# Kernel tuning notes

Hardware: AMD Instinct MI355X
Metric: run time of the kernel (lower is better)

Reference implementation:

```python
import jax, jax.numpy as jnp
import numpy as np

BN_EPS = 1e-5


def setup_inputs() -> dict:
    N, E, D, L = 100000, 1200000, 64, 3
    key = jax.random.key(0)
    ks = jax.random.split(key, 6)
    x = jax.random.normal(ks[0], (N, D), dtype=jnp.float32)
    src = jax.random.randint(ks[1], (E,), 0, N, dtype=jnp.int32)
    dst = jax.random.randint(ks[2], (E,), 0, N, dtype=jnp.int32)
    W1 = jax.random.normal(ks[3], (L, D, D), dtype=jnp.float32) * 0.1
    W2 = jax.random.normal(ks[4], (L, D, D), dtype=jnp.float32) * 0.1
    b1 = jnp.zeros((L, D), jnp.float32)
    b2 = jnp.zeros((L, D), jnp.float32)
    bn_gamma = jnp.ones((L, D), jnp.float32)
    bn_beta = jnp.zeros((L, D), jnp.float32)
    bn_mean = jnp.zeros((L, D), jnp.float32)
    bn_var = jnp.ones((L, D), jnp.float32)
    return {"x": x, "src": src, "dst": dst, "W1": W1, "b1": b1,
            "bn_gamma": bn_gamma, "bn_beta": bn_beta, "bn_mean": bn_mean,
            "bn_var": bn_var, "W2": W2, "b2": b2}


def reference(x, src, dst, W1, b1, bn_gamma, bn_beta, bn_mean, bn_var, W2, b2):
    # GIN stack, eval mode (dropout is a no-op, BatchNorm uses running stats).
    N = x.shape[0]
    L = W1.shape[0]
    h = x
    jk_sum = jnp.zeros((N, W2.shape[-1]), x.dtype)
    for layer in range(L):  # small fixed layer loop
        # GINConv with eps=0: (1+eps)*x_i + sum_{j->i} x_j
        agg = jax.ops.segment_sum(h[src], dst, num_segments=N)  # [N, D]
        pre = h + agg
        # MLP: Linear -> BatchNorm1d (inference) -> ReLU -> Linear
        z = pre @ W1[layer] + b1[layer]
        z = bn_gamma[layer] * (z - bn_mean[layer]) * jax.lax.rsqrt(bn_var[layer] + BN_EPS) + bn_beta[layer]
        z = jax.nn.relu(z)
        h = z @ W2[layer] + b2[layer]
        if layer != L - 1:
            h = jax.nn.relu(h)  # inter-layer ReLU from the wrapper
        jk_sum = jk_sum + h  # JK='sum' over h_list[1:]
    return jk_sum
```

## Files before the change

### kernel.cpp

```cpp
#include <hip/hip_runtime.h>
#include <hip/hip_fp16.h>

#define NDIM 64
#define RS 68
#define MAXNB 512
#define CAP 6144
#define EBUF 352

typedef _Float16 h4 __attribute__((ext_vector_type(4)));
typedef float f4v __attribute__((ext_vector_type(4)));

__global__ __launch_bounds__(256) void prep_kernel(
    const float* __restrict__ x, __half* __restrict__ x16, int n4,
    const float* __restrict__ W1, const float* __restrict__ b1,
    const float* __restrict__ gamma, const float* __restrict__ beta,
    const float* __restrict__ mean, const float* __restrict__ var,
    const float* __restrict__ W2,
    _Float16* __restrict__ Wpk, float* __restrict__ b1f, int L,
    int* __restrict__ bcnt, int nbz)
{
    int bid = blockIdx.x;
    int t = threadIdx.x;
    if (bid < 2 * L) {
        if (bid == 0)
            for (int i = t; i < nbz; i += 256) bcnt[i] = 0;
        int l = bid >> 1, m = bid & 1;
        const float* Wsrc = (m == 0 ? W1 : W2) + (size_t)l * 4096;
        if (m == 0 && t < 64) {
            float s = gamma[l * 64 + t] * rsqrtf(var[l * 64 + t] + 1e-5f);
            b1f[l * 64 + t] = (b1[l * 64 + t] - mean[l * 64 + t]) * s + beta[l * 64 + t];
        }
        int lane = t & 63;
        int c16 = lane & 15, kq = lane >> 4;
        for (int it = 0; it < 4; ++it) {
            int frag = it * 4 + (t >> 6);
            int ks = frag >> 2, ct = frag & 3;
            int col = ct * 16 + c16;
            int k0 = ks * 16 + kq * 4;
            float s = 1.f;
            if (m == 0) s = gamma[l * 64 + col] * rsqrtf(var[l * 64 + col] + 1e-5f);
            _Float16* dstp = Wpk + (((size_t)(l * 2 + m) * 16 + frag) * 64 + lane) * 8;
            for (int j = 0; j < 4; ++j) {
                float wv = Wsrc[(size_t)(k0 + j) * 64 + col] * s;
                _Float16 hi = (_Float16)wv;
                dstp[j] = hi;
                dstp[4 + j] = (_Float16)(wv - (float)hi);
            }
        }
        return;
    }
    int tid = (bid - 2 * L) * 256 + t;
    if (tid >= n4) return;
    float4 v = *(const float4*)(x + (size_t)tid * 4);
    __half2* dp = (__half2*)(x16 + (size_t)tid * 4);
    dp[0] = __floats2half2_rn(v.x, v.y);
    dp[1] = __floats2half2_rn(v.z, v.w);
}

__global__ __launch_bounds__(256) void bucket_scatter_kernel(
    const int* __restrict__ src, const int* __restrict__ dst,
    int* __restrict__ bcnt, unsigned int* __restrict__ packed, int E, int NBb)
{
    __shared__ int hist[MAXNB];
    __shared__ int sbase[MAXNB];
    for (int i = threadIdx.x; i < NBb; i += 256) hist[i] = 0;
    __syncthreads();
    int start = blockIdx.x * blockDim.x + threadIdx.x;
    int stride = gridDim.x * blockDim.x;
    for (int e = start; e < E; e += stride)
        atomicAdd(&hist[dst[e] >> 8], 1);
    __syncthreads();
    for (int i = threadIdx.x; i < NBb; i += 256) {
        int v = hist[i];
        sbase[i] = v ? (i * CAP + atomicAdd(&bcnt[i], v)) : 0;
    }
    __syncthreads();
    for (int i = threadIdx.x; i < NBb; i += 256) hist[i] = 0;
    __syncthreads();
    for (int e = start; e < E; e += stride) {
        int d = dst[e];
        int b = d >> 8;
        int r = atomicAdd(&hist[b], 1);
        packed[sbase[b] + r] = (unsigned)src[e] | ((unsigned)(d & 255) << 24);
    }
}

__global__ __launch_bounds__(256) void bucket_csr_kernel(
    const unsigned int* __restrict__ packed, const int* __restrict__ bcnt,
    int* __restrict__ ssrc, int* __restrict__ offs, int* __restrict__ ends, int N)
{
    __shared__ int hist[256], scan[256], cur[256];
    __shared__ int swbase;
    int b = blockIdx.x;
    int t = threadIdx.x;
    int partial = 0;
    for (int i = t; i < b; i += 256) partial += bcnt[i];
    scan[t] = partial;
    hist[t] = 0;
    __syncthreads();
    for (int d = 128; d > 0; d >>= 1) {
        if (t < d) scan[t] += scan[t + d];
        __syncthreads();
    }
    if (t == 0) swbase = scan[0];
    __syncthreads();
    int wbase = swbase;
    int cnt = bcnt[b];
    if (cnt > CAP) cnt = CAP;
    size_t rbase = (size_t)b * CAP;
    for (int i = t; i < cnt; i += 256)
        atomicAdd(&hist[packed[rbase + i] >> 24], 1);
    __syncthreads();
    int v = hist[t];
    scan[t] = v;
    __syncthreads();
    for (int d = 1; d < 256; d <<= 1) {
        int x = scan[t];
        int y = (t >= d) ? scan[t - d] : 0;
        __syncthreads();
        scan[t] = x + y;
        __syncthreads();
    }
    int e0 = wbase + scan[t] - v;
    cur[t] = e0;
    int node = b * 256 + t;
    if (node < N) { offs[node] = e0; ends[node] = e0 + v; }
    __syncthreads();
    for (int i = t; i < cnt; i += 256) {
        unsigned p = packed[rbase + i];
        int pos = atomicAdd(&cur[p >> 24], 1);
        ssrc[pos] = (int)(p & 0xFFFFFF);
    }
}

__device__ inline void add4(float4& a, const float4& v) {
    a.x += v.x; a.y += v.y; a.z += v.z; a.w += v.w;
}

__device__ inline void cvt_acc(uint4 u, float4& a0, float4& a1) {
    __half2 h0 = __builtin_bit_cast(__half2, u.x);
    __half2 h1 = __builtin_bit_cast(__half2, u.y);
    __half2 h2 = __builtin_bit_cast(__half2, u.z);
    __half2 h3 = __builtin_bit_cast(__half2, u.w);
    float2 f0 = __half22float2(h0), f1 = __half22float2(h1);
    float2 f2 = __half22float2(h2), f3 = __half22float2(h3);
    a0.x += f0.x; a0.y += f0.y; a0.z += f1.x; a0.w += f1.y;
    a1.x += f2.x; a1.y += f2.y; a1.z += f3.x; a1.w += f3.y;
}

__global__ __launch_bounds__(256, 7) void gin_layer_kernel(
    const __half* __restrict__ hin, __half* __restrict__ hout,
    float* __restrict__ jk, const __half* __restrict__ hbase,
    const int* __restrict__ offs, const int* __restrict__ ends,
    const int* __restrict__ ssrc,
    const _Float16* __restrict__ w1p, const _Float16* __restrict__ w2p,
    const float* __restrict__ b1f, const float* __restrict__ b2,
    int N, int L, int relu_out, int last)
{
    __shared__ float lds[64 * RS];
    __shared__ int ebuf_s[4 * EBUF];
    int t = threadIdx.x;
    int lane = t & 63;
    int w = t >> 6;
    int row0 = blockIdx.x * 64;
    int wrow0 = row0 + w * 16;
    if (wrow0 >= N) return;

    float* wtile = lds + (size_t)w * 16 * RS;
    int* ebuf = ebuf_s + w * EBUF;

    int offv = 0, endv = 0;
    if (lane < 16) {
        int node = wrow0 + lane;
        int cn = (node < N) ? node : (N - 1);
        offv = offs[cn];
        endv = ends[cn];
        if (node >= N) offv = endv;
    }
    int begAll = __shfl(offv, 0, 64);
    int endAll = __shfl(endv, 15, 64);
    int cnt = endAll - begAll;

    bool useLds = (cnt <= EBUF);
    if (useLds) {
        for (int k = lane; k < cnt; k += 64) ebuf[k] = ssrc[begAll + k];
    }
    asm volatile("" ::: "memory");
    auto eidx = [&](int pos) -> int {
        return useLds ? ebuf[pos - begAll] : ssrc[pos];
    };

    {
        int rslot = lane >> 3;
        int q = lane & 7;
        int nodeA = wrow0 + rslot;
        int nodeB = wrow0 + 8 + rslot;
        int begA = __shfl(offv, rslot, 64),     endA = __shfl(endv, rslot, 64);
        int begB = __shfl(offv, 8 + rslot, 64), endB = __shfl(endv, 8 + rslot, 64);

        float4 a0 = make_float4(0.f, 0.f, 0.f, 0.f);
        float4 a1 = make_float4(0.f, 0.f, 0.f, 0.f);
        float4 c0 = make_float4(0.f, 0.f, 0.f, 0.f);
        float4 c1 = make_float4(0.f, 0.f, 0.f, 0.f);
        if (nodeA < N) {
            uint4 u = *(const uint4*)(hin + (size_t)nodeA * NDIM + q * 8);
            cvt_acc(u, a0, a1);
        }
        if (nodeB < N) {
            uint4 u = *(const uint4*)(hin + (size_t)nodeB * NDIM + q * 8);
            cvt_acc(u, c0, c1);
        }
        int kA = begA, kB = begB;
        while (kA + 2 <= endA && kB + 2 <= endB) {
            int iA0 = eidx(kA), iA1 = eidx(kA + 1);
            int iB0 = eidx(kB), iB1 = eidx(kB + 1);
            uint4 uA0 = *(const uint4*)(hin + (size_t)iA0 * NDIM + q * 8);
            uint4 uA1 = *(const uint4*)(hin + (size_t)iA1 * NDIM + q * 8);
            uint4 uB0 = *(const uint4*)(hin + (size_t)iB0 * NDIM + q * 8);
            uint4 uB1 = *(const uint4*)(hin + (size_t)iB1 * NDIM + q * 8);
            cvt_acc(uA0, a0, a1);
            cvt_acc(uA1, a0, a1);
            cvt_acc(uB0, c0, c1);
            cvt_acc(uB1, c0, c1);
            kA += 2; kB += 2;
        }
        for (; kA < endA; ++kA) {
            uint4 u = *(const uint4*)(hin + (size_t)eidx(kA) * NDIM + q * 8);
            cvt_acc(u, a0, a1);
        }
        for (; kB < endB; ++kB) {
            uint4 u = *(const uint4*)(hin + (size_t)eidx(kB) * NDIM + q * 8);
            cvt_acc(u, c0, c1);
        }
        if (nodeA < N) {
            float* p = wtile + rslot * RS + q * 8;
            *(float4*)(p) = a0;
            *(float4*)(p + 4) = a1;
        }
        if (nodeB < N) {
            float* p = wtile + (8 + rslot) * RS + q * 8;
            *(float4*)(p) = c0;
            *(float4*)(p + 4) = c1;
        }
    }
    asm volatile("" ::: "memory");

    int lane15 = lane & 15;
    int lgrp = lane >> 4;
    const float* aRow = wtile + (size_t)lane15 * RS;
    const h4* W1 = (const h4*)w1p;
    const h4* W2 = (const h4*)w2p;
    f4v zero = {0.f, 0.f, 0.f, 0.f};
    f4v acc[4];

    #pragma unroll
    for (int ct = 0; ct < 4; ++ct) acc[ct] = zero;
    #pragma unroll
    for (int ks = 0; ks < 4; ++ks) {
        float4 av = *(const float4*)(aRow + ks * 16 + lgrp * 4);
        h4 ah, al;
        ah[0] = (_Float16)av.x; al[0] = (_Float16)(av.x - (float)ah[0]);
        ah[1] = (_Float16)av.y; al[1] = (_Float16)(av.y - (float)ah[1]);
        ah[2] = (_Float16)av.z; al[2] = (_Float16)(av.z - (float)ah[2]);
        ah[3] = (_Float16)av.w; al[3] = (_Float16)(av.w - (float)ah[3]);
        #pragma unroll
        for (int ct = 0; ct < 4; ++ct) {
            const h4* bp = W1 + (size_t)((ks * 4 + ct) * 64 + lane) * 2;
            h4 bh = bp[0], bl = bp[1];
            acc[ct] = __builtin_amdgcn_mfma_f32_16x16x16f16(ah, bh, acc[ct], 0, 0, 0);
            acc[ct] = __builtin_amdgcn_mfma_f32_16x16x16f16(al, bh, acc[ct], 0, 0, 0);
            acc[ct] = __builtin_amdgcn_mfma_f32_16x16x16f16(ah, bl, acc[ct], 0, 0, 0);
        }
    }
    asm volatile("" ::: "memory");
    #pragma unroll
    for (int ct = 0; ct < 4; ++ct) {
        int col = ct * 16 + lane15;
        float bb = b1f[col];
        #pragma unroll
        for (int i = 0; i < 4; ++i)
            wtile[(size_t)(lgrp * 4 + i) * RS + col] = fmaxf(acc[ct][i] + bb, 0.f);
    }
    asm volatile("" ::: "memory");

    #pragma unroll
    for (int ct = 0; ct < 4; ++ct) acc[ct] = zero;
    #pragma unroll
    for (int ks = 0; ks < 4; ++ks) {
        float4 av = *(const float4*)(aRow + ks * 16 + lgrp * 4);
        h4 ah, al;
        ah[0] = (_Float16)av.x; al[0] = (_Float16)(av.x - (float)ah[0]);
        ah[1] = (_Float16)av.y; al[1] = (_Float16)(av.y - (float)ah[1]);
        ah[2] = (_Float16)av.z; al[2] = (_Float16)(av.z - (float)ah[2]);
        ah[3] = (_Float16)av.w; al[3] = (_Float16)(av.w - (float)ah[3]);
        #pragma unroll
        for (int ct = 0; ct < 4; ++ct) {
            const h4* bp = W2 + (size_t)((ks * 4 + ct) * 64 + lane) * 2;
            h4 bh = bp[0], bl = bp[1];
            acc[ct] = __builtin_amdgcn_mfma_f32_16x16x16f16(ah, bh, acc[ct], 0, 0, 0);
            acc[ct] = __builtin_amdgcn_mfma_f32_16x16x16f16(al, bh, acc[ct], 0, 0, 0);
            acc[ct] = __builtin_amdgcn_mfma_f32_16x16x16f16(ah, bl, acc[ct], 0, 0, 0);
        }
    }
    asm volatile("" ::: "memory");
    #pragma unroll
    for (int ct = 0; ct < 4; ++ct) {
        int col = ct * 16 + lane15;
        float bb = b2[col];
        #pragma unroll
        for (int i = 0; i < 4; ++i) {
            float hv = acc[ct][i] + bb;
            if (relu_out) hv = fmaxf(hv, 0.f);
            wtile[(size_t)(lgrp * 4 + i) * RS + col] = hv;
        }
    }
    asm volatile("" ::: "memory");

    size_t nstride = (size_t)N * NDIM;
    #pragma unroll
    for (int it = 0; it < 4; ++it) {
        int fl = it * 64 + lane;
        int r = fl >> 4, c4 = fl & 15;
        int grow = wrow0 + r;
        if (grow >= N) continue;
        const float* p = wtile + (size_t)r * RS + c4 * 4;
        float4 hv = make_float4(p[0], p[1], p[2], p[3]);
        if (!last) {
            __half2* dp = (__half2*)(hout + (size_t)grow * NDIM + c4 * 4);
            dp[0] = __floats2half2_rn(hv.x, hv.y);
            dp[1] = __floats2half2_rn(hv.z, hv.w);
        } else {
            for (int j = 1; j < L; ++j) {
                uint2 u = *(const uint2*)(hbase + (size_t)j * nstride
                                          + (size_t)grow * NDIM + c4 * 4);
                __half2 x0 = __builtin_bit_cast(__half2, u.x);
                __half2 x1 = __builtin_bit_cast(__half2, u.y);
                float2 f0 = __half22float2(x0), f1 = __half22float2(x1);
                hv.x += f0.x; hv.y += f0.y; hv.z += f1.x; hv.w += f1.y;
            }
            *(float4*)(jk + (size_t)grow * NDIM + c4 * 4) = hv;
        }
    }
}

extern "C" void kernel_launch(void* const* d_in, const int* in_sizes, int n_in,
                              void* d_out, int out_size, void* d_ws, size_t ws_size,
                              hipStream_t stream) {
    const float* x     = (const float*)d_in[0];
    const int*   src   = (const int*)  d_in[1];
    const int*   dst   = (const int*)  d_in[2];
    const float* W1    = (const float*)d_in[3];
    const float* b1    = (const float*)d_in[4];
    const float* gamma = (const float*)d_in[5];
    const float* beta  = (const float*)d_in[6];
    const float* mean  = (const float*)d_in[7];
    const float* var   = (const float*)d_in[8];
    const float* W2    = (const float*)d_in[9];
    const float* b2    = (const float*)d_in[10];

    int N = in_sizes[0] / NDIM;
    int E = in_sizes[1];
    int L = in_sizes[3] / (NDIM * NDIM);
    int NBb = (N + 255) >> 8;
    int n4 = N * NDIM / 4;
    float* out = (float*)d_out;
    size_t ns = (size_t)N * NDIM;

    char* w = (char*)d_ws;
    size_t off = 0;
    auto carve = [&](size_t bytes) -> void* {
        void* p = w + off;
        off += (bytes + 255) & ~(size_t)255;
        return p;
    };
    __half* h16     = (__half*)carve((size_t)(L + 1) * ns * 2);
    int*    ssrc    = (int*)   carve((size_t)E * 4);
    unsigned int* packed = (unsigned int*)carve((size_t)NBb * CAP * 4);
    int*    offs    = (int*)   carve((size_t)N * 4);
    int*    ends    = (int*)   carve((size_t)N * 4);
    int*    bcnt    = (int*)   carve((size_t)(MAXNB + 1) * 4);
    _Float16* Wpk   = (_Float16*)carve((size_t)L * 2 * 16 * 64 * 8 * 2);
    float*  b1f     = (float*) carve((size_t)L * NDIM * 4);

    prep_kernel<<<2 * L + (n4 + 255) / 256, 256, 0, stream>>>(
        x, h16, n4, W1, b1, gamma, beta, mean, var, W2, Wpk, b1f, L,
        bcnt, NBb + 1);
    bucket_scatter_kernel<<<256, 256, 0, stream>>>(src, dst, bcnt, packed, E, NBb);
    bucket_csr_kernel<<<NBb, 256, 0, stream>>>(packed, bcnt, ssrc, offs, ends, N);

    for (int l = 0; l < L; ++l) {
        gin_layer_kernel<<<(N + 63) / 64, 256, 0, stream>>>(
            h16 + (size_t)l * ns, h16 + (size_t)(l + 1) * ns, out, h16,
            offs, ends, ssrc,
            Wpk + (size_t)(l * 2 + 0) * 16 * 64 * 8,
            Wpk + (size_t)(l * 2 + 1) * 16 * 64 * 8,
            b1f + (size_t)l * NDIM, b2 + (size_t)l * NDIM,
            N, L, (l < L - 1) ? 1 : 0, (l == L - 1) ? 1 : 0);
    }
}
```

Measured before the change: 244.4 us.

## Use one-wavefront blocks per 16 rows and unroll gather loop by four

The GIN layer kernel now launches 64-thread blocks that each own 16 rows, instead of 256-thread blocks holding four independent waves. Each block's shared memory shrinks to one wave's tile and edge buffer. This removes tail imbalance inside a block, since a wave no longer waits on its siblings before the block's resources are freed. The neighbor-gather loop is also unrolled to four edges per row pair, with a two-edge remainder, to put more loads in flight. In exchange there are four times as many blocks, and the extra live registers could limit occupancy.

```diff
diff --git a/kernel.cpp b/kernel.cpp
--- a/kernel.cpp
+++ b/kernel.cpp
@@ -148,7 +148,7 @@
     a1.x += f2.x; a1.y += f2.y; a1.z += f3.x; a1.w += f3.y;
 }
 
-__global__ __launch_bounds__(256, 7) void gin_layer_kernel(
+__global__ __launch_bounds__(64, 7) void gin_layer_kernel(
     const __half* __restrict__ hin, __half* __restrict__ hout,
     float* __restrict__ jk, const __half* __restrict__ hbase,
     const int* __restrict__ offs, const int* __restrict__ ends,
@@ -157,17 +157,11 @@
     const float* __restrict__ b1f, const float* __restrict__ b2,
     int N, int L, int relu_out, int last)
 {
-    __shared__ float lds[64 * RS];
-    __shared__ int ebuf_s[4 * EBUF];
-    int t = threadIdx.x;
-    int lane = t & 63;
-    int w = t >> 6;
-    int row0 = blockIdx.x * 64;
-    int wrow0 = row0 + w * 16;
+    __shared__ float wtile[16 * RS];
+    __shared__ int ebuf[EBUF];
+    int lane = threadIdx.x;
+    int wrow0 = blockIdx.x * 16;
     if (wrow0 >= N) return;
-
-    float* wtile = lds + (size_t)w * 16 * RS;
-    int* ebuf = ebuf_s + w * EBUF;
 
     int offv = 0, endv = 0;
     if (lane < 16) {
@@ -211,24 +205,42 @@
             cvt_acc(u, c0, c1);
         }
         int kA = begA, kB = begB;
-        while (kA + 2 <= endA && kB + 2 <= endB) {
-            int iA0 = eidx(kA), iA1 = eidx(kA + 1);
-            int iB0 = eidx(kB), iB1 = eidx(kB + 1);
+        while (kA + 4 <= endA && kB + 4 <= endB) {
+            int iA0 = eidx(kA), iA1 = eidx(kA + 1), iA2 = eidx(kA + 2), iA3 = eidx(kA + 3);
+            int iB0 = eidx(kB), iB1 = eidx(kB + 1), iB2 = eidx(kB + 2), iB3 = eidx(kB + 3);
             uint4 uA0 = *(const uint4*)(hin + (size_t)iA0 * NDIM + q * 8);
             uint4 uA1 = *(const uint4*)(hin + (size_t)iA1 * NDIM + q * 8);
+            uint4 uA2 = *(const uint4*)(hin + (size_t)iA2 * NDIM + q * 8);
+            uint4 uA3 = *(const uint4*)(hin + (size_t)iA3 * NDIM + q * 8);
             uint4 uB0 = *(const uint4*)(hin + (size_t)iB0 * NDIM + q * 8);
             uint4 uB1 = *(const uint4*)(hin + (size_t)iB1 * NDIM + q * 8);
-            cvt_acc(uA0, a0, a1);
-            cvt_acc(uA1, a0, a1);
-            cvt_acc(uB0, c0, c1);
-            cvt_acc(uB1, c0, c1);
-            kA += 2; kB += 2;
-        }
-        for (; kA < endA; ++kA) {
+            uint4 uB2 = *(const uint4*)(hin + (size_t)iB2 * NDIM + q * 8);
+            uint4 uB3 = *(const uint4*)(hin + (size_t)iB3 * NDIM + q * 8);
+            cvt_acc(uA0, a0, a1); cvt_acc(uA1, a0, a1);
+            cvt_acc(uA2, a0, a1); cvt_acc(uA3, a0, a1);
+            cvt_acc(uB0, c0, c1); cvt_acc(uB1, c0, c1);
+            cvt_acc(uB2, c0, c1); cvt_acc(uB3, c0, c1);
+            kA += 4; kB += 4;
+        }
+        for (; kA + 2 <= endA; kA += 2) {
+            int i0 = eidx(kA), i1 = eidx(kA + 1);
+            uint4 u0 = *(const uint4*)(hin + (size_t)i0 * NDIM + q * 8);
+            uint4 u1 = *(const uint4*)(hin + (size_t)i1 * NDIM + q * 8);
+            cvt_acc(u0, a0, a1);
+            cvt_acc(u1, a0, a1);
+        }
+        if (kA < endA) {
             uint4 u = *(const uint4*)(hin + (size_t)eidx(kA) * NDIM + q * 8);
             cvt_acc(u, a0, a1);
         }
-        for (; kB < endB; ++kB) {
+        for (; kB + 2 <= endB; kB += 2) {
+            int i0 = eidx(kB), i1 = eidx(kB + 1);
+            uint4 u0 = *(const uint4*)(hin + (size_t)i0 * NDIM + q * 8);
+            uint4 u1 = *(const uint4*)(hin + (size_t)i1 * NDIM + q * 8);
+            cvt_acc(u0, c0, c1);
+            cvt_acc(u1, c0, c1);
+        }
+        if (kB < endB) {
             uint4 u = *(const uint4*)(hin + (size_t)eidx(kB) * NDIM + q * 8);
             cvt_acc(u, c0, c1);
         }
@@ -388,8 +400,9 @@
     bucket_scatter_kernel<<<256, 256, 0, stream>>>(src, dst, bcnt, packed, E, NBb);
     bucket_csr_kernel<<<NBb, 256, 0, stream>>>(packed, bcnt, ssrc, offs, ends, N);
 
+    int NB16 = (N + 15) / 16;
     for (int l = 0; l < L; ++l) {
-        gin_layer_kernel<<<(N + 63) / 64, 256, 0, stream>>>(
+        gin_layer_kernel<<<NB16, 64, 0, stream>>>(
             h16 + (size_t)l * ns, h16 + (size_t)(l + 1) * ns, out, h16,
             offs, ends, ssrc,
             Wpk + (size_t)(l * 2 + 0) * 16 * 64 * 8,
```

After: 234.5 us (median of 2 runs). -4.1%, faster.
